# Kernel tuning notes

Measured on AMD Instinct MI355X. Metric: run time of the kernel, lower is better.

Reference implementation:

```python
import jax, jax.numpy as jnp
import numpy as np

B, LP, LE, D, H, DK, DV, DF = 16, 2047, 2048, 1024, 16, 64, 64, 4096


def _layer_norm(x, g, b, eps=1e-5):
    m = x.mean(-1, keepdims=True)
    v = ((x - m) ** 2).mean(-1, keepdims=True)
    return (x - m) * jax.lax.rsqrt(v + eps) * g + b


def _mha(q, kv, wq, wk, wv, wo, bo, g, b):
    # q: [B,Q,D], kv: [B,L,D]; per-head projections wq/wk: [H,D,DK], wv: [H,D,DV]
    residual = q
    Q = jnp.einsum('bqd,hdk->bhqk', q, wq)
    K = jnp.einsum('bld,hdk->bhlk', kv, wk)
    V = jnp.einsum('bld,hdv->bhlv', kv, wv)
    scale = jnp.sqrt(jnp.asarray(Q.shape[-1], Q.dtype))
    attn = jax.nn.softmax(jnp.einsum('bhqk,bhlk->bhql', Q, K) / scale, axis=-1)
    o = jnp.einsum('bhql,bhlv->bhqv', attn, V)
    o = o.transpose(0, 2, 1, 3).reshape(q.shape[0], q.shape[1], -1)  # concat heads
    o = o @ wo + bo
    return _layer_norm(o + residual, g, b), attn


def setup_inputs() -> dict:
    key = jax.random.key(0)
    ks = jax.random.split(key, 16)
    s = 0.02
    inp = {
        'dec_input': jax.random.normal(ks[0], (B, 1, D), jnp.float32),
        'input_history': jax.random.normal(ks[1], (B, LP, D), jnp.float32),
        'enc_output': jax.random.normal(ks[2], (B, LE, D), jnp.float32),
        'wq_s': jax.random.normal(ks[3], (H, D, DK), jnp.float32) * s,
        'wk_s': jax.random.normal(ks[4], (H, D, DK), jnp.float32) * s,
        'wv_s': jax.random.normal(ks[5], (H, D, DV), jnp.float32) * s,
        'wo_s': jax.random.normal(ks[6], (H * DV, D), jnp.float32) * s,
        'bo_s': jnp.zeros((D,), jnp.float32),
        'ln1_g': jnp.ones((D,), jnp.float32),
        'ln1_b': jnp.zeros((D,), jnp.float32),
        'wq_c': jax.random.normal(ks[7], (H, D, DK), jnp.float32) * s,
        'wk_c': jax.random.normal(ks[8], (H, D, DK), jnp.float32) * s,
        'wv_c': jax.random.normal(ks[9], (H, D, DV), jnp.float32) * s,
        'wo_c': jax.random.normal(ks[10], (H * DV, D), jnp.float32) * s,
        'bo_c': jnp.zeros((D,), jnp.float32),
        'ln2_g': jnp.ones((D,), jnp.float32),
        'ln2_b': jnp.zeros((D,), jnp.float32),
        'ffn_w1': jax.random.normal(ks[11], (D, DF), jnp.float32) * s,
        'ffn_b1': jnp.zeros((DF,), jnp.float32),
        'ffn_w2': jax.random.normal(ks[12], (DF, D), jnp.float32) * s,
        'ffn_b2': jnp.zeros((D,), jnp.float32),
        'ln3_g': jnp.ones((D,), jnp.float32),
        'ln3_b': jnp.zeros((D,), jnp.float32),
    }
    return inp


def reference(dec_input, input_history, enc_output,
              wq_s, wk_s, wv_s, wo_s, bo_s, ln1_g, ln1_b,
              wq_c, wk_c, wv_c, wo_c, bo_c, ln2_g, ln2_b,
              ffn_w1, ffn_b1, ffn_w2, ffn_b2, ln3_g, ln3_b):
    # KV-cache growth: history <- cat(history, dec_input)
    history = jnp.concatenate([input_history, dec_input], axis=1)  # [B, LP+1, D]
    x, slf_attn = _mha(dec_input, history, wq_s, wk_s, wv_s, wo_s, bo_s, ln1_g, ln1_b)
    x, enc_attn = _mha(x, enc_output, wq_c, wk_c, wv_c, wo_c, bo_c, ln2_g, ln2_b)
    y = jax.nn.relu(x @ ffn_w1 + ffn_b1) @ ffn_w2 + ffn_b2
    out = _layer_norm(y + x, ln3_g, ln3_b)
    return (out, slf_attn, enc_attn)
```

## Files before the change

### kernel.cpp

```cpp
#include <hip/hip_runtime.h>
#include <hip/hip_bf16.h>
#include <stdint.h>
#include <stddef.h>


#define DEV __device__ __forceinline__

typedef __attribute__((ext_vector_type(8))) short bf16x8;
typedef __attribute__((ext_vector_type(4))) float f32x4;

DEV unsigned short f2b(float f){
  union { __hip_bfloat16 h; unsigned short u; } cv;
  cv.h = __float2bfloat16(f);
  return cv.u;
}
DEV f32x4 mfma16(bf16x8 a, bf16x8 b, f32x4 c){
  return __builtin_amdgcn_mfma_f32_16x16x32_bf16(a, b, c, 0, 0, 0);
}
DEV float4 fma4(float4 a, float s, float4 b){
  a.x += s*b.x; a.y += s*b.y; a.z += s*b.z; a.w += s*b.w; return a;
}

__global__ __launch_bounds__(256) void k_qp2(const float* __restrict__ src,
    const float* __restrict__ wq, const float* __restrict__ wk,
    unsigned short* __restrict__ qpb){
  int bh = blockIdx.x, b = bh >> 4, h = bh & 15;
  int t = threadIdx.x;
  __shared__ float red[256];
  __shared__ float Qs[64];
  {
    int k = t & 63, q = t >> 6;
    const float* s = src + (size_t)b*1024 + q*256;
    const float* w = wq + (size_t)h*65536 + (size_t)(q*256)*64 + k;
    float a0=0.f,a1=0.f,a2=0.f,a3=0.f;
    for(int d=0; d<256; d+=4){
      a0 += s[d]   * w[(size_t)d*64];
      a1 += s[d+1] * w[(size_t)(d+1)*64];
      a2 += s[d+2] * w[(size_t)(d+2)*64];
      a3 += s[d+3] * w[(size_t)(d+3)*64];
    }
    red[t] = a0+a1+a2+a3;
    __syncthreads();
    if(t < 64) Qs[t] = (red[t]+red[t+64]+red[t+128]+red[t+192])*0.125f;
    __syncthreads();
  }
  for(int i=0;i<4;++i){
    int d = t + i*256;
    const float* w = wk + ((size_t)h*1024 + d)*64;
    float acc = 0.f;
    #pragma unroll
    for(int k4=0;k4<16;++k4){
      float4 wv4 = *(const float4*)(w + k4*4);
      acc += wv4.x*Qs[k4*4] + wv4.y*Qs[k4*4+1] + wv4.z*Qs[k4*4+2] + wv4.w*Qs[k4*4+3];
    }
    qpb[(size_t)bh*1024 + d] = f2b(acc);
  }
}

__global__ __launch_bounds__(256) void k_attn(const float* __restrict__ kvsrc,
    const float* __restrict__ decrow, const unsigned short* __restrict__ qpb,
    float* __restrict__ scr, float* __restrict__ part, float* __restrict__ msum,
    int lsrc){
  int ns = blockIdx.x, b = blockIdx.y;
  int t = threadIdx.x, lane = t & 63, w = t >> 6;
  int r = lane & 15, hi = lane >> 4;
  int slice0 = ns*64;

  __shared__ unsigned short lt[1024*24];
  __shared__ float red[4*64*4];
  __shared__ unsigned short p_lds[16*40];
  __shared__ float f_lds[16];

  float4 ld[16];
  auto ISSUE = [&](int c){
    int row = slice0 + c*16 + r;
    const float* rp = (row < lsrc) ? kvsrc + ((size_t)b*lsrc + row)*1024
                                   : decrow + (size_t)b*1024;
    rp += w*256 + hi*8;
    #pragma unroll
    for(int kk=0; kk<8; ++kk){
      ld[kk*2+0] = *(const float4*)(rp + kk*32);
      ld[kk*2+1] = *(const float4*)(rp + kk*32 + 4);
    }
  };

  ISSUE(0);
  for(int i=t; i<16*40; i+=256) p_lds[i] = 0;

  bf16x8 qf[8];
  {
    const unsigned short* qp = qpb + ((size_t)b*16 + r)*1024 + w*256 + hi*8;
    #pragma unroll
    for(int kk=0;kk<8;++kk) qf[kk] = *(const bf16x8*)(qp + kk*32);
  }

  f32x4 acc[16];
  #pragma unroll
  for(int i=0;i<16;++i) acc[i] = (f32x4){0.f,0.f,0.f,0.f};
  float m_run = -1e30f, s_run = 0.f;

  __syncthreads();
  for(int c=0; c<4; ++c){
    f32x4 s_acc = {0.f,0.f,0.f,0.f};
    int colw = r ^ ((hi & 1) << 3);
    #pragma unroll
    for(int kk=0; kk<8; ++kk){
      float4 a0 = ld[kk*2], a1 = ld[kk*2+1];
      bf16x8 v;
      v[0]=(short)f2b(a0.x); v[1]=(short)f2b(a0.y);
      v[2]=(short)f2b(a0.z); v[3]=(short)f2b(a0.w);
      v[4]=(short)f2b(a1.x); v[5]=(short)f2b(a1.y);
      v[6]=(short)f2b(a1.z); v[7]=(short)f2b(a1.w);
      unsigned short* pt = &lt[(w*256 + hi*8 + kk*32)*24 + colw];
      #pragma unroll
      for(int j=0;j<8;++j) pt[j*24] = (unsigned short)v[j];
      s_acc = mfma16(v, qf[kk], s_acc);
    }
    if(c < 3) ISSUE(c+1);
    *(f32x4*)&red[t*4] = s_acc;
    __syncthreads();

    f32x4 ss = *(const f32x4*)&red[(0*64+lane)*4];
    ss += *(const f32x4*)&red[(1*64+lane)*4];
    ss += *(const f32x4*)&red[(2*64+lane)*4];
    ss += *(const f32x4*)&red[(3*64+lane)*4];
    float sf[4] = {ss[0], ss[1], ss[2], ss[3]};
    float mc = fmaxf(fmaxf(sf[0],sf[1]), fmaxf(sf[2],sf[3]));
    mc = fmaxf(mc, __shfl_xor(mc, 16));
    mc = fmaxf(mc, __shfl_xor(mc, 32));
    float nm = fmaxf(m_run, mc);
    float fch = __expf(m_run - nm);
    float pvv[4]; float ps = 0.f;
    #pragma unroll
    for(int i=0;i<4;++i){ pvv[i] = __expf(sf[i]-nm); ps += pvv[i]; }
    ps += __shfl_xor(ps, 16);
    ps += __shfl_xor(ps, 32);
    s_run = s_run*fch + ps;
    m_run = nm;
    if(w == 0){
      #pragma unroll
      for(int i=0;i<4;++i) p_lds[r*40 + hi*4 + i] = f2b(pvv[i]);
      if(hi == 0) f_lds[r] = fch;
      float* sp = scr + ((size_t)b*16 + r)*2048 + slice0 + c*16 + hi*4;
      *(float4*)sp = (float4){sf[0], sf[1], sf[2], sf[3]};
    }
    __syncthreads();

    f32x4 fv = *(const f32x4*)&f_lds[hi*4];
    bf16x8 pa = *(const bf16x8*)&p_lds[r*40 + hi*8];
    #pragma unroll
    for(int dc=0; dc<16; ++dc){
      acc[dc] *= fv;
      int d = w*256 + dc*16 + r;
      int col0 = (((hi & 1) ^ ((r >> 3) & 1)) << 3);
      bf16x8 bv = *(const bf16x8*)&lt[d*24 + col0];
      acc[dc] = mfma16(pa, bv, acc[dc]);
    }
    __syncthreads();
  }
  float* pp = part + (((size_t)b*32 + ns)*16)*1024 + w*256 + r;
  #pragma unroll
  for(int dc=0; dc<16; ++dc)
    #pragma unroll
    for(int i=0;i<4;++i)
      pp[(size_t)(hi*4+i)*1024 + dc*16] = acc[dc][i];
  if(w==0 && hi==0){
    msum[(((size_t)b*32 + ns)*16 + r)*2 + 0] = m_run;
    msum[(((size_t)b*32 + ns)*16 + r)*2 + 1] = s_run;
  }
}

__global__ __launch_bounds__(256) void k_fin(const float* __restrict__ part,
    const float* __restrict__ msum, const float* __restrict__ scr,
    const float* __restrict__ wv, float* __restrict__ attn_out,
    unsigned short* __restrict__ ob){
  int bh = blockIdx.x, b = bh >> 4, h = bh & 15;
  int t = threadIdx.x;
  __shared__ float marr[32], earr[32], ctxs[1024], red2[256];
  if(t < 32){
    marr[t] = msum[(((size_t)b*32 + t)*16 + h)*2 + 0];
    earr[t] = msum[(((size_t)b*32 + t)*16 + h)*2 + 1];
  }
  __syncthreads();
  float M = -1e30f;
  for(int i=0;i<32;++i) M = fmaxf(M, marr[i]);
  float SUM = 0.f;
  for(int i=0;i<32;++i) SUM += __expf(marr[i]-M)*earr[i];
  float inv = 1.f/SUM;
  __syncthreads();
  if(t < 32) earr[t] = __expf(marr[t]-M)*inv;
  __syncthreads();
  {
    const float4* p4 = (const float4*)part + ((size_t)b*32*16 + h)*256 + t;
    float4 a = {0.f,0.f,0.f,0.f};
    #pragma unroll 4
    for(int nsq=0; nsq<32; ++nsq) a = fma4(a, earr[nsq], p4[(size_t)nsq*4096]);
    *(float4*)&ctxs[t*4] = a;
  }
  const float* sp = scr + ((size_t)b*16 + h)*2048;
  float* po = attn_out + ((size_t)b*16 + h)*2048;
  #pragma unroll
  for(int i=0;i<8;++i){ int l = t + i*256; po[l] = __expf(sp[l]-M)*inv; }
  __syncthreads();
  int v = t & 63, q = t >> 6;
  const float* wp = wv + ((size_t)h*1024 + q*256)*64 + v;
  float a0=0.f,a1=0.f,a2=0.f,a3=0.f;
  for(int dd=0; dd<256; dd+=4){
    a0 += ctxs[q*256+dd]   * wp[(size_t)dd*64];
    a1 += ctxs[q*256+dd+1] * wp[(size_t)(dd+1)*64];
    a2 += ctxs[q*256+dd+2] * wp[(size_t)(dd+2)*64];
    a3 += ctxs[q*256+dd+3] * wp[(size_t)(dd+3)*64];
  }
  red2[t] = a0+a1+a2+a3;
  __syncthreads();
  if(t < 64)
    ob[(size_t)b*1024 + h*64 + t] = f2b(red2[t]+red2[t+64]+red2[t+128]+red2[t+192]);
}

__global__ __launch_bounds__(256) void k_skgemm(const float* __restrict__ W,
    const unsigned short* __restrict__ A, float* __restrict__ part,
    int N, int K, int KS){
  int nt = blockIdx.x, ks = blockIdx.y;
  int Ksl = K / KS, k0b = ks * Ksl, n0 = nt*64;
  int nc = Ksl >> 5;
  __shared__ unsigned short lt[2][64*40];
  int t = threadIdx.x, lane = t & 63, w = t >> 6;
  int k_loc = t >> 3, n_off = (t & 7)*8;
  const unsigned short* apb = A + (size_t)(lane & 15)*K + (lane >> 4)*8 + k0b;
  f32x4 acc = {0.f,0.f,0.f,0.f};
  float4 x0, x1;
  auto LD = [&](int c){
    const float* wp = W + (size_t)(k0b + c*32 + k_loc)*N + n0 + n_off;
    x0 = *(const float4*)wp;
    x1 = *(const float4*)(wp + 4);
  };
  auto ST = [&](int buf){
    unsigned short* p = &lt[buf][0];
    p[(n_off+0)*40 + k_loc] = f2b(x0.x);
    p[(n_off+1)*40 + k_loc] = f2b(x0.y);
    p[(n_off+2)*40 + k_loc] = f2b(x0.z);
    p[(n_off+3)*40 + k_loc] = f2b(x0.w);
    p[(n_off+4)*40 + k_loc] = f2b(x1.x);
    p[(n_off+5)*40 + k_loc] = f2b(x1.y);
    p[(n_off+6)*40 + k_loc] = f2b(x1.z);
    p[(n_off+7)*40 + k_loc] = f2b(x1.w);
  };
  LD(0); ST(0);
  for(int c=0; c<nc; ++c){
    if(c+1 < nc) LD(c+1);
    __syncthreads();
    bf16x8 af = *(const bf16x8*)(apb + c*32);
    bf16x8 bv = *(const bf16x8*)&lt[c&1][(w*16 + (lane & 15))*40 + (lane >> 4)*8];
    acc = mfma16(af, bv, acc);
    if(c+1 < nc) ST((c+1)&1);
  }
  int col = n0 + w*16 + (lane & 15);
  int r0 = (lane >> 4)*4;
  #pragma unroll
  for(int i=0;i<4;++i)
    part[ ((size_t)ks*16 + r0 + i)*(size_t)N + col ] = acc[i];
}

__global__ __launch_bounds__(256) void k_lnres(const float* __restrict__ parts, int KS,
    const float* __restrict__ bias, const float* __restrict__ resid,
    const float* __restrict__ g, const float* __restrict__ bb,
    float* __restrict__ xout, unsigned short* __restrict__ xb16){
  int b = blockIdx.x, t = threadIdx.x;
  __shared__ float red[256];
  const float4* bias4  = (const float4*)bias;
  const float4* resid4 = (const float4*)resid + (size_t)b*256;
  const float4* parts4 = (const float4*)parts;
  float4 s = bias4[t];
  { float4 rr = resid4[t]; s.x+=rr.x; s.y+=rr.y; s.z+=rr.z; s.w+=rr.w; }
  #pragma unroll 4
  for(int k=0;k<KS;++k){
    float4 pp = parts4[((size_t)k*16 + b)*256 + t];
    s.x+=pp.x; s.y+=pp.y; s.z+=pp.z; s.w+=pp.w;
  }
  red[t] = s.x+s.y+s.z+s.w; __syncthreads();
  for(int off=128; off>0; off>>=1){ if(t<off) red[t]+=red[t+off]; __syncthreads(); }
  float mean = red[0]*(1.f/1024.f); __syncthreads();
  float dx=s.x-mean, dy=s.y-mean, dz=s.z-mean, dw=s.w-mean;
  red[t] = dx*dx+dy*dy+dz*dz+dw*dw; __syncthreads();
  for(int off=128; off>0; off>>=1){ if(t<off) red[t]+=red[t+off]; __syncthreads(); }
  float rstd = rsqrtf(red[0]*(1.f/1024.f) + 1e-5f);
  float4 g4 = ((const float4*)g)[t], b4 = ((const float4*)bb)[t];
  float4 y;
  y.x = dx*rstd*g4.x + b4.x;
  y.y = dy*rstd*g4.y + b4.y;
  y.z = dz*rstd*g4.z + b4.z;
  y.w = dw*rstd*g4.w + b4.w;
  if(xout) ((float4*)xout)[(size_t)b*256 + t] = y;
  if(xb16){
    ushort4 u;
    u.x = f2b(y.x); u.y = f2b(y.y); u.z = f2b(y.z); u.w = f2b(y.w);
    ((ushort4*)xb16)[(size_t)b*256 + t] = u;
  }
}

__global__ __launch_bounds__(256) void k_relu(const float* __restrict__ parts, int KS,
    const float* __restrict__ b1, unsigned short* __restrict__ h1){
  int i = blockIdx.x*256 + threadIdx.x;
  int b = i >> 10, f4 = i & 1023;
  float4 s = ((const float4*)b1)[f4];
  #pragma unroll 4
  for(int k=0;k<KS;++k){
    float4 pp = ((const float4*)parts)[((size_t)k*16 + b)*1024 + f4];
    s.x+=pp.x; s.y+=pp.y; s.z+=pp.z; s.w+=pp.w;
  }
  ushort4 u;
  u.x = f2b(fmaxf(s.x,0.f)); u.y = f2b(fmaxf(s.y,0.f));
  u.z = f2b(fmaxf(s.z,0.f)); u.w = f2b(fmaxf(s.w,0.f));
  ((ushort4*)h1)[i] = u;
}

extern "C" void kernel_launch(void* const* d_in, const int* in_sizes, int n_in,
                              void* d_out, int out_size, void* d_ws, size_t ws_size,
                              hipStream_t stream){
  const float* dec    = (const float*)d_in[0];
  const float* hist   = (const float*)d_in[1];
  const float* enc    = (const float*)d_in[2];
  const float* wq_s   = (const float*)d_in[3];
  const float* wk_s   = (const float*)d_in[4];
  const float* wv_s   = (const float*)d_in[5];
  const float* wo_s   = (const float*)d_in[6];
  const float* bo_s   = (const float*)d_in[7];
  const float* ln1_g  = (const float*)d_in[8];
  const float* ln1_b  = (const float*)d_in[9];
  const float* wq_c   = (const float*)d_in[10];
  const float* wk_c   = (const float*)d_in[11];
  const float* wv_c   = (const float*)d_in[12];
  const float* wo_c   = (const float*)d_in[13];
  const float* bo_c   = (const float*)d_in[14];
  const float* ln2_g  = (const float*)d_in[15];
  const float* ln2_b  = (const float*)d_in[16];
  const float* ffn_w1 = (const float*)d_in[17];
  const float* ffn_b1 = (const float*)d_in[18];
  const float* ffn_w2 = (const float*)d_in[19];
  const float* ffn_b2 = (const float*)d_in[20];
  const float* ln3_g  = (const float*)d_in[21];
  const float* ln3_b  = (const float*)d_in[22];

  float* out      = (float*)d_out;
  float* slf_out  = out + 16384;
  float* enc_out  = out + 16384 + 524288;

  char* w = (char*)d_ws;
  float*          scr   = (float*)(w + 0x0000000);
  float*          part  = (float*)(w + 0x0200000);
  float*          msum  = (float*)(w + 0x2200000);
  unsigned short* qpb   = (unsigned short*)(w + 0x2210000);
  unsigned short* ob    = (unsigned short*)(w + 0x2290000);
  float*          x1    = (float*)(w + 0x22A0000);
  float*          x2    = (float*)(w + 0x22B0000);
  unsigned short* x2b   = (unsigned short*)(w + 0x22C0000);
  unsigned short* h1b   = (unsigned short*)(w + 0x22D0000);
  float*          gpart = (float*)(w + 0x2300000);
  float*          fpart = (float*)(w + 0x2400000);
  float*          g2part= (float*)(w + 0x2600000);

  k_qp2   <<<256, 256, 0, stream>>>(dec, wq_s, wk_s, qpb);
  k_attn  <<<dim3(32,16), 256, 0, stream>>>(hist, dec, qpb, scr, part, msum, 2047);
  k_fin   <<<256, 256, 0, stream>>>(part, msum, scr, wv_s, slf_out, ob);
  k_skgemm<<<dim3(16,16), 256, 0, stream>>>(wo_s, ob, gpart, 1024, 1024, 16);
  k_lnres <<<16, 256, 0, stream>>>(gpart, 16, bo_s, dec, ln1_g, ln1_b, x1, (unsigned short*)nullptr);

  k_qp2   <<<256, 256, 0, stream>>>(x1, wq_c, wk_c, qpb);
  k_attn  <<<dim3(32,16), 256, 0, stream>>>(enc, dec, qpb, scr, part, msum, 2048);
  k_fin   <<<256, 256, 0, stream>>>(part, msum, scr, wv_c, enc_out, ob);
  k_skgemm<<<dim3(16,16), 256, 0, stream>>>(wo_c, ob, gpart, 1024, 1024, 16);
  k_lnres <<<16, 256, 0, stream>>>(gpart, 16, bo_c, x1, ln2_g, ln2_b, x2, x2b);

  k_skgemm<<<dim3(64,8), 256, 0, stream>>>(ffn_w1, x2b, fpart, 4096, 1024, 8);
  k_relu  <<<64, 256, 0, stream>>>(fpart, 8, ffn_b1, h1b);
  k_skgemm<<<dim3(16,32), 256, 0, stream>>>(ffn_w2, h1b, g2part, 1024, 4096, 32);
  k_lnres <<<16, 256, 0, stream>>>(g2part, 32, ffn_b2, x2, ln3_g, ln3_b, out, (unsigned short*)nullptr);
}
```

Before: 197.3 us.

## Split attention into finer slices, store bf16 partials, fuse output projection into finalize

Each attention block now covers 32 KV rows instead of 64, so 1024 blocks are launched instead of 512, with a smaller LDS tile that uses stride-20 padding. Per-slice context partials are staged through LDS and written as bf16 rather than fp32, which halves partial write/read traffic at some precision cost. The finalize kernel now also applies the per-head slice of the output projection and writes per-head partials for the layernorm kernel to reduce, removing the separate split-K GEMM launch. The fused projection is a plain scalar loop over 64 weight rows per block, which may be slower than the dedicated GEMM it replaces.

```diff
diff --git a/kernel.cpp b/kernel.cpp
--- a/kernel.cpp
+++ b/kernel.cpp
@@ -7,6 +7,7 @@
 #define DEV __device__ __forceinline__
 
 typedef __attribute__((ext_vector_type(8))) short bf16x8;
+typedef __attribute__((ext_vector_type(4))) short bf16x4;
 typedef __attribute__((ext_vector_type(4))) float f32x4;
 
 DEV unsigned short f2b(float f){
@@ -14,17 +15,19 @@
   cv.h = __float2bfloat16(f);
   return cv.u;
 }
+DEV float b2f(unsigned short u){
+  union { unsigned int i; float f; } cv;
+  cv.i = ((unsigned int)u) << 16;
+  return cv.f;
+}
 DEV f32x4 mfma16(bf16x8 a, bf16x8 b, f32x4 c){
   return __builtin_amdgcn_mfma_f32_16x16x32_bf16(a, b, c, 0, 0, 0);
 }
-DEV float4 fma4(float4 a, float s, float4 b){
-  a.x += s*b.x; a.y += s*b.y; a.z += s*b.z; a.w += s*b.w; return a;
-}
-
-__global__ __launch_bounds__(256) void k_qp2(const float* __restrict__ src,
+
+__global__ __launch_bounds__(256) void g_qp2(const float* __restrict__ src,
     const float* __restrict__ wq, const float* __restrict__ wk,
     unsigned short* __restrict__ qpb){
-  int bh = blockIdx.x, b = bh >> 4, h = bh & 15;
+  int u = blockIdx.x, b = u >> 4, h = u & 15;
   int t = threadIdx.x;
   __shared__ float red[256];
   __shared__ float Qs[64];
@@ -53,21 +56,21 @@
       float4 wv4 = *(const float4*)(w + k4*4);
       acc += wv4.x*Qs[k4*4] + wv4.y*Qs[k4*4+1] + wv4.z*Qs[k4*4+2] + wv4.w*Qs[k4*4+3];
     }
-    qpb[(size_t)bh*1024 + d] = f2b(acc);
-  }
-}
-
-__global__ __launch_bounds__(256) void k_attn(const float* __restrict__ kvsrc,
+    qpb[(size_t)u*1024 + d] = f2b(acc);
+  }
+}
+
+__global__ __launch_bounds__(256) void g_attn(const float* __restrict__ kvsrc,
     const float* __restrict__ decrow, const unsigned short* __restrict__ qpb,
-    float* __restrict__ scr, float* __restrict__ part, float* __restrict__ msum,
-    int lsrc){
-  int ns = blockIdx.x, b = blockIdx.y;
+    float* __restrict__ scr, unsigned short* __restrict__ partb,
+    float* __restrict__ msum, int lsrc){
+  int u = blockIdx.x, ns = u & 63, b = u >> 6;
   int t = threadIdx.x, lane = t & 63, w = t >> 6;
   int r = lane & 15, hi = lane >> 4;
-  int slice0 = ns*64;
-
-  __shared__ unsigned short lt[1024*24];
-  __shared__ float red[4*64*4];
+  int slice0 = ns*32;
+
+  __shared__ unsigned short lt[1024*20];
+  __shared__ float red[1024];
   __shared__ unsigned short p_lds[16*40];
   __shared__ float f_lds[16];
 
@@ -100,7 +103,7 @@
   float m_run = -1e30f, s_run = 0.f;
 
   __syncthreads();
-  for(int c=0; c<4; ++c){
+  for(int c=0; c<2; ++c){
     f32x4 s_acc = {0.f,0.f,0.f,0.f};
     int colw = r ^ ((hi & 1) << 3);
     #pragma unroll
@@ -111,12 +114,12 @@
       v[2]=(short)f2b(a0.z); v[3]=(short)f2b(a0.w);
       v[4]=(short)f2b(a1.x); v[5]=(short)f2b(a1.y);
       v[6]=(short)f2b(a1.z); v[7]=(short)f2b(a1.w);
-      unsigned short* pt = &lt[(w*256 + hi*8 + kk*32)*24 + colw];
+      unsigned short* pt = &lt[(w*256 + hi*8 + kk*32)*20 + colw];
       #pragma unroll
-      for(int j=0;j<8;++j) pt[j*24] = (unsigned short)v[j];
+      for(int j=0;j<8;++j) pt[j*20] = (unsigned short)v[j];
       s_acc = mfma16(v, qf[kk], s_acc);
     }
-    if(c < 3) ISSUE(c+1);
+    if(c < 1) ISSUE(c+1);
     *(f32x4*)&red[t*4] = s_acc;
     __syncthreads();
 
@@ -153,49 +156,63 @@
       acc[dc] *= fv;
       int d = w*256 + dc*16 + r;
       int col0 = (((hi & 1) ^ ((r >> 3) & 1)) << 3);
-      bf16x8 bv = *(const bf16x8*)&lt[d*24 + col0];
+      bf16x4 blo = *(const bf16x4*)&lt[d*20 + col0];
+      bf16x4 bhi = *(const bf16x4*)&lt[d*20 + col0 + 4];
+      bf16x8 bv;
+      bv[0]=blo[0]; bv[1]=blo[1]; bv[2]=blo[2]; bv[3]=blo[3];
+      bv[4]=bhi[0]; bv[5]=bhi[1]; bv[6]=bhi[2]; bv[7]=bhi[3];
       acc[dc] = mfma16(pa, bv, acc[dc]);
     }
     __syncthreads();
   }
-  float* pp = part + (((size_t)b*32 + ns)*16)*1024 + w*256 + r;
+  unsigned short* pl = lt;
   #pragma unroll
   for(int dc=0; dc<16; ++dc)
     #pragma unroll
     for(int i=0;i<4;++i)
-      pp[(size_t)(hi*4+i)*1024 + dc*16] = acc[dc][i];
+      pl[(hi*4+i)*1024 + w*256 + dc*16 + r] = f2b(acc[dc][i]);
+  __syncthreads();
+  {
+    const uint4* s4 = (const uint4*)pl;
+    uint4* d4 = (uint4*)(partb + (((size_t)b*64 + ns)*16)*1024);
+    #pragma unroll
+    for(int j=0;j<8;++j) d4[t + j*256] = s4[t + j*256];
+  }
   if(w==0 && hi==0){
-    msum[(((size_t)b*32 + ns)*16 + r)*2 + 0] = m_run;
-    msum[(((size_t)b*32 + ns)*16 + r)*2 + 1] = s_run;
-  }
-}
-
-__global__ __launch_bounds__(256) void k_fin(const float* __restrict__ part,
+    msum[(((size_t)b*64 + ns)*16 + r)*2 + 0] = m_run;
+    msum[(((size_t)b*64 + ns)*16 + r)*2 + 1] = s_run;
+  }
+}
+
+__global__ __launch_bounds__(256) void g_fin(const unsigned short* __restrict__ partb,
     const float* __restrict__ msum, const float* __restrict__ scr,
-    const float* __restrict__ wv, float* __restrict__ attn_out,
-    unsigned short* __restrict__ ob){
-  int bh = blockIdx.x, b = bh >> 4, h = bh & 15;
+    const float* __restrict__ wv, const float* __restrict__ wo,
+    float* __restrict__ attn_out, float* __restrict__ gpart){
+  int u = blockIdx.x, b = u >> 4, h = u & 15;
   int t = threadIdx.x;
-  __shared__ float marr[32], earr[32], ctxs[1024], red2[256];
-  if(t < 32){
-    marr[t] = msum[(((size_t)b*32 + t)*16 + h)*2 + 0];
-    earr[t] = msum[(((size_t)b*32 + t)*16 + h)*2 + 1];
+  __shared__ float marr[64], earr[64], ctxs[1024], red2[256], obh[64];
+  if(t < 64){
+    marr[t] = msum[(((size_t)b*64 + t)*16 + h)*2 + 0];
+    earr[t] = msum[(((size_t)b*64 + t)*16 + h)*2 + 1];
   }
   __syncthreads();
   float M = -1e30f;
-  for(int i=0;i<32;++i) M = fmaxf(M, marr[i]);
+  for(int i=0;i<64;++i) M = fmaxf(M, marr[i]);
   float SUM = 0.f;
-  for(int i=0;i<32;++i) SUM += __expf(marr[i]-M)*earr[i];
+  for(int i=0;i<64;++i) SUM += __expf(marr[i]-M)*earr[i];
   float inv = 1.f/SUM;
   __syncthreads();
-  if(t < 32) earr[t] = __expf(marr[t]-M)*inv;
+  if(t < 64) earr[t] = __expf(marr[t]-M)*inv;
   __syncthreads();
   {
-    const float4* p4 = (const float4*)part + ((size_t)b*32*16 + h)*256 + t;
-    float4 a = {0.f,0.f,0.f,0.f};
-    #pragma unroll 4
-    for(int nsq=0; nsq<32; ++nsq) a = fma4(a, earr[nsq], p4[(size_t)nsq*4096]);
-    *(float4*)&ctxs[t*4] = a;
+    const unsigned short* pb0 = partb + ((size_t)b*64*16 + h)*1024 + t*4;
+    float ax=0.f, ay=0.f, az=0.f, aw=0.f;
+    for(int nsq=0; nsq<64; ++nsq){
+      ushort4 uu = *(const ushort4*)(pb0 + (size_t)nsq*16384);
+      float e = earr[nsq];
+      ax += e*b2f(uu.x); ay += e*b2f(uu.y); az += e*b2f(uu.z); aw += e*b2f(uu.w);
+    }
+    *(float4*)&ctxs[t*4] = (float4){ax,ay,az,aw};
   }
   const float* sp = scr + ((size_t)b*16 + h)*2048;
   float* po = attn_out + ((size_t)b*16 + h)*2048;
@@ -213,11 +230,58 @@
   }
   red2[t] = a0+a1+a2+a3;
   __syncthreads();
-  if(t < 64)
-    ob[(size_t)b*1024 + h*64 + t] = f2b(red2[t]+red2[t+64]+red2[t+128]+red2[t+192]);
-}
-
-__global__ __launch_bounds__(256) void k_skgemm(const float* __restrict__ W,
+  if(t < 64) obh[t] = red2[t]+red2[t+64]+red2[t+128]+red2[t+192];
+  __syncthreads();
+  float accn[4] = {0.f,0.f,0.f,0.f};
+  const float* wrow = wo + (size_t)h*64*1024;
+  for(int vv=0; vv<64; ++vv){
+    float s = obh[vv];
+    const float* wr = wrow + (size_t)vv*1024;
+    #pragma unroll
+    for(int i=0;i<4;++i) accn[i] += s * wr[t + i*256];
+  }
+  #pragma unroll
+  for(int i=0;i<4;++i) gpart[((size_t)h*16 + b)*1024 + t + i*256] = accn[i];
+}
+
+__global__ __launch_bounds__(256) void g_ln(const float* __restrict__ parts, int KS,
+    const float* __restrict__ bias, const float* __restrict__ resid,
+    const float* __restrict__ g, const float* __restrict__ bb,
+    float* __restrict__ xout, unsigned short* __restrict__ xb16){
+  int b = blockIdx.x, t = threadIdx.x;
+  __shared__ float red[256];
+  const float4* bias4  = (const float4*)bias;
+  const float4* resid4 = (const float4*)resid + (size_t)b*256;
+  const float4* parts4 = (const float4*)parts;
+  float4 s = bias4[t];
+  { float4 rr = resid4[t]; s.x+=rr.x; s.y+=rr.y; s.z+=rr.z; s.w+=rr.w; }
+  #pragma unroll 4
+  for(int k=0;k<KS;++k){
+    float4 pp = parts4[((size_t)k*16 + b)*256 + t];
+    s.x+=pp.x; s.y+=pp.y; s.z+=pp.z; s.w+=pp.w;
+  }
+  red[t] = s.x+s.y+s.z+s.w; __syncthreads();
+  for(int off=128; off>0; off>>=1){ if(t<off) red[t]+=red[t+off]; __syncthreads(); }
+  float mean = red[0]*(1.f/1024.f); __syncthreads();
+  float dx=s.x-mean, dy=s.y-mean, dz=s.z-mean, dw=s.w-mean;
+  red[t] = dx*dx+dy*dy+dz*dz+dw*dw; __syncthreads();
+  for(int off=128; off>0; off>>=1){ if(t<off) red[t]+=red[t+off]; __syncthreads(); }
+  float rstd = rsqrtf(red[0]*(1.f/1024.f) + 1e-5f);
+  float4 g4 = ((const float4*)g)[t], b4 = ((const float4*)bb)[t];
+  float4 y;
+  y.x = dx*rstd*g4.x + b4.x;
+  y.y = dy*rstd*g4.y + b4.y;
+  y.z = dz*rstd*g4.z + b4.z;
+  y.w = dw*rstd*g4.w + b4.w;
+  if(xout) ((float4*)xout)[(size_t)b*256 + t] = y;
+  if(xb16){
+    ushort4 uu;
+    uu.x = f2b(y.x); uu.y = f2b(y.y); uu.z = f2b(y.z); uu.w = f2b(y.w);
+    ((ushort4*)xb16)[(size_t)b*256 + t] = uu;
+  }
+}
+
+__global__ __launch_bounds__(256) void g_skg(const float* __restrict__ W,
     const unsigned short* __restrict__ A, float* __restrict__ part,
     int N, int K, int KS){
   int nt = blockIdx.x, ks = blockIdx.y;
@@ -261,44 +325,7 @@
     part[ ((size_t)ks*16 + r0 + i)*(size_t)N + col ] = acc[i];
 }
 
-__global__ __launch_bounds__(256) void k_lnres(const float* __restrict__ parts, int KS,
-    const float* __restrict__ bias, const float* __restrict__ resid,
-    const float* __restrict__ g, const float* __restrict__ bb,
-    float* __restrict__ xout, unsigned short* __restrict__ xb16){
-  int b = blockIdx.x, t = threadIdx.x;
-  __shared__ float red[256];
-  const float4* bias4  = (const float4*)bias;
-  const float4* resid4 = (const float4*)resid + (size_t)b*256;
-  const float4* parts4 = (const float4*)parts;
-  float4 s = bias4[t];
-  { float4 rr = resid4[t]; s.x+=rr.x; s.y+=rr.y; s.z+=rr.z; s.w+=rr.w; }
-  #pragma unroll 4
-  for(int k=0;k<KS;++k){
-    float4 pp = parts4[((size_t)k*16 + b)*256 + t];
-    s.x+=pp.x; s.y+=pp.y; s.z+=pp.z; s.w+=pp.w;
-  }
-  red[t] = s.x+s.y+s.z+s.w; __syncthreads();
-  for(int off=128; off>0; off>>=1){ if(t<off) red[t]+=red[t+off]; __syncthreads(); }
-  float mean = red[0]*(1.f/1024.f); __syncthreads();
-  float dx=s.x-mean, dy=s.y-mean, dz=s.z-mean, dw=s.w-mean;
-  red[t] = dx*dx+dy*dy+dz*dz+dw*dw; __syncthreads();
-  for(int off=128; off>0; off>>=1){ if(t<off) red[t]+=red[t+off]; __syncthreads(); }
-  float rstd = rsqrtf(red[0]*(1.f/1024.f) + 1e-5f);
-  float4 g4 = ((const float4*)g)[t], b4 = ((const float4*)bb)[t];
-  float4 y;
-  y.x = dx*rstd*g4.x + b4.x;
-  y.y = dy*rstd*g4.y + b4.y;
-  y.z = dz*rstd*g4.z + b4.z;
-  y.w = dw*rstd*g4.w + b4.w;
-  if(xout) ((float4*)xout)[(size_t)b*256 + t] = y;
-  if(xb16){
-    ushort4 u;
-    u.x = f2b(y.x); u.y = f2b(y.y); u.z = f2b(y.z); u.w = f2b(y.w);
-    ((ushort4*)xb16)[(size_t)b*256 + t] = u;
-  }
-}
-
-__global__ __launch_bounds__(256) void k_relu(const float* __restrict__ parts, int KS,
+__global__ __launch_bounds__(256) void g_relu(const float* __restrict__ parts, int KS,
     const float* __restrict__ b1, unsigned short* __restrict__ h1){
   int i = blockIdx.x*256 + threadIdx.x;
   int b = i >> 10, f4 = i & 1023;
@@ -308,10 +335,10 @@
     float4 pp = ((const float4*)parts)[((size_t)k*16 + b)*1024 + f4];
     s.x+=pp.x; s.y+=pp.y; s.z+=pp.z; s.w+=pp.w;
   }
-  ushort4 u;
-  u.x = f2b(fmaxf(s.x,0.f)); u.y = f2b(fmaxf(s.y,0.f));
-  u.z = f2b(fmaxf(s.z,0.f)); u.w = f2b(fmaxf(s.w,0.f));
-  ((ushort4*)h1)[i] = u;
+  ushort4 uu;
+  uu.x = f2b(fmaxf(s.x,0.f)); uu.y = f2b(fmaxf(s.y,0.f));
+  uu.z = f2b(fmaxf(s.z,0.f)); uu.w = f2b(fmaxf(s.w,0.f));
+  ((ushort4*)h1)[i] = uu;
 }
 
 extern "C" void kernel_launch(void* const* d_in, const int* in_sizes, int n_in,
@@ -334,45 +361,42 @@
   const float* bo_c   = (const float*)d_in[14];
   const float* ln2_g  = (const float*)d_in[15];
   const float* ln2_b  = (const float*)d_in[16];
-  const float* ffn_w1 = (const float*)d_in[17];
-  const float* ffn_b1 = (const float*)d_in[18];
-  const float* ffn_w2 = (const float*)d_in[19];
-  const float* ffn_b2 = (const float*)d_in[20];
+  const float* w1     = (const float*)d_in[17];
+  const float* b1     = (const float*)d_in[18];
+  const float* w2     = (const float*)d_in[19];
+  const float* b2     = (const float*)d_in[20];
   const float* ln3_g  = (const float*)d_in[21];
   const float* ln3_b  = (const float*)d_in[22];
 
-  float* out      = (float*)d_out;
-  float* slf_out  = out + 16384;
-  float* enc_out  = out + 16384 + 524288;
+  float* out  = (float*)d_out;
+  float* slf  = out + 16384;
+  float* enco = out + 16384 + 524288;
 
   char* w = (char*)d_ws;
-  float*          scr   = (float*)(w + 0x0000000);
-  float*          part  = (float*)(w + 0x0200000);
-  float*          msum  = (float*)(w + 0x2200000);
-  unsigned short* qpb   = (unsigned short*)(w + 0x2210000);
-  unsigned short* ob    = (unsigned short*)(w + 0x2290000);
-  float*          x1    = (float*)(w + 0x22A0000);
-  float*          x2    = (float*)(w + 0x22B0000);
-  unsigned short* x2b   = (unsigned short*)(w + 0x22C0000);
-  unsigned short* h1b   = (unsigned short*)(w + 0x22D0000);
-  float*          gpart = (float*)(w + 0x2300000);
-  float*          fpart = (float*)(w + 0x2400000);
-  float*          g2part= (float*)(w + 0x2600000);
-
-  k_qp2   <<<256, 256, 0, stream>>>(dec, wq_s, wk_s, qpb);
-  k_attn  <<<dim3(32,16), 256, 0, stream>>>(hist, dec, qpb, scr, part, msum, 2047);
-  k_fin   <<<256, 256, 0, stream>>>(part, msum, scr, wv_s, slf_out, ob);
-  k_skgemm<<<dim3(16,16), 256, 0, stream>>>(wo_s, ob, gpart, 1024, 1024, 16);
-  k_lnres <<<16, 256, 0, stream>>>(gpart, 16, bo_s, dec, ln1_g, ln1_b, x1, (unsigned short*)nullptr);
-
-  k_qp2   <<<256, 256, 0, stream>>>(x1, wq_c, wk_c, qpb);
-  k_attn  <<<dim3(32,16), 256, 0, stream>>>(enc, dec, qpb, scr, part, msum, 2048);
-  k_fin   <<<256, 256, 0, stream>>>(part, msum, scr, wv_c, enc_out, ob);
-  k_skgemm<<<dim3(16,16), 256, 0, stream>>>(wo_c, ob, gpart, 1024, 1024, 16);
-  k_lnres <<<16, 256, 0, stream>>>(gpart, 16, bo_c, x1, ln2_g, ln2_b, x2, x2b);
-
-  k_skgemm<<<dim3(64,8), 256, 0, stream>>>(ffn_w1, x2b, fpart, 4096, 1024, 8);
-  k_relu  <<<64, 256, 0, stream>>>(fpart, 8, ffn_b1, h1b);
-  k_skgemm<<<dim3(16,32), 256, 0, stream>>>(ffn_w2, h1b, g2part, 1024, 4096, 32);
-  k_lnres <<<16, 256, 0, stream>>>(g2part, 32, ffn_b2, x2, ln3_g, ln3_b, out, (unsigned short*)nullptr);
-}
+  float*          scr    = (float*)(w + 0x0000000);
+  unsigned short* partb  = (unsigned short*)(w + 0x0200000);
+  float*          msum   = (float*)(w + 0x2200000);
+  unsigned short* qpb    = (unsigned short*)(w + 0x2240000);
+  float*          x1     = (float*)(w + 0x22C0000);
+  float*          x2     = (float*)(w + 0x22D0000);
+  unsigned short* x2b    = (unsigned short*)(w + 0x22E0000);
+  unsigned short* h1b    = (unsigned short*)(w + 0x22F0000);
+  float*          gpart  = (float*)(w + 0x2400000);
+  float*          fpart  = (float*)(w + 0x2500000);
+  float*          g2part = (float*)(w + 0x2700000);
+
+  g_qp2 <<<256,  256, 0, stream>>>(dec, wq_s, wk_s, qpb);
+  g_attn<<<1024, 256, 0, stream>>>(hist, dec, qpb, scr, partb, msum, 2047);
+  g_fin <<<256,  256, 0, stream>>>(partb, msum, scr, wv_s, wo_s, slf, gpart);
+  g_ln  <<<16,   256, 0, stream>>>(gpart, 16, bo_s, dec, ln1_g, ln1_b, x1, (unsigned short*)0);
+
+  g_qp2 <<<256,  256, 0, stream>>>(x1, wq_c, wk_c, qpb);
+  g_attn<<<1024, 256, 0, stream>>>(enc, dec, qpb, scr, partb, msum, 2048);
+  g_fin <<<256,  256, 0, stream>>>(partb, msum, scr, wv_c, wo_c, enco, gpart);
+  g_ln  <<<16,   256, 0, stream>>>(gpart, 16, bo_c, x1, ln2_g, ln2_b, x2, x2b);
+
+  g_skg <<<dim3(64,8),  256, 0, stream>>>(w1, x2b, fpart, 4096, 1024, 8);
+  g_relu<<<64,  256, 0, stream>>>(fpart, 8, b1, h1b);
+  g_skg <<<dim3(16,32), 256, 0, stream>>>(w2, h1b, g2part, 1024, 4096, 32);
+  g_ln  <<<16,  256, 0, stream>>>(g2part, 32, b2, x2, ln3_g, ln3_b, out, (unsigned short*)0);
+}
```

Result: no change. 194.7 us (-1.3%).
